# Optimization experiments

Hardware: AMD Instinct MI355X
Metric: run time of the kernel (lower is better)

## Reference

```python
import jax, jax.numpy as jnp
import numpy as np

N_NODES = 100000
N_EDGES = 1600000
IN, HID, OUT = 128, 128, 64


def setup_inputs() -> dict:
    key = jax.random.key(0)
    ks = jax.random.split(key, 6)
    features = jax.random.normal(ks[0], (N_NODES, IN), dtype=jnp.float32)
    src = jax.random.randint(ks[1], (N_EDGES,), 0, N_NODES)
    dst = jax.random.randint(ks[2], (N_EDGES,), 0, N_NODES)
    # Glorot-style init scales
    W1 = jax.random.normal(ks[3], (IN, HID), dtype=jnp.float32) * (1.0 / np.sqrt(IN))
    b1 = jnp.zeros((HID,), dtype=jnp.float32)
    W2 = jax.random.normal(ks[4], (HID, OUT), dtype=jnp.float32) * (1.0 / np.sqrt(HID))
    b2 = jnp.zeros((OUT,), dtype=jnp.float32)
    return {"features": features, "src": src, "dst": dst,
            "W1": W1, "b1": b1, "W2": W2, "b2": b2}


def _graph_conv(h, W, b, src, dst, deg_inv):
    # DGL GraphConv, norm='right': aggregate sum of (x_u W) over in-neighbors,
    # divide by in-degree (clamped to >=1), then add bias.
    m = h @ W                                   # [N, F_out]
    agg = jax.ops.segment_sum(m[src], dst, num_segments=h.shape[0])  # [N, F_out]
    return agg * deg_inv[:, None] + b


def reference(features, src, dst, W1, b1, W2, b2):
    n = features.shape[0]
    deg = jax.ops.segment_sum(jnp.ones_like(dst, dtype=features.dtype), dst,
                              num_segments=n)
    deg_inv = 1.0 / jnp.maximum(deg, 1.0)       # clamp(min=1) as in DGL
    h = jax.nn.relu(_graph_conv(features, W1, b1, src, dst, deg_inv))
    # dropout(0.5) is identity in eval mode
    out = _graph_conv(h, W2, b2, src, dst, deg_inv)
    return out
```

## Files before the change

kernel.cpp:

```cpp
#include <hip/hip_runtime.h>
#include <hip/hip_fp16.h>


constexpr int CAP = 3072;
constexpr int CHUNK = 8192;

typedef _Float16 f16x8 __attribute__((ext_vector_type(8)));
typedef float f32x4 __attribute__((ext_vector_type(4)));

__global__ __launch_bounds__(256) void k_prep(
    const int* __restrict__ dst, int* __restrict__ counts,
    const float* __restrict__ W1, const float* __restrict__ W2,
    __half* __restrict__ W1t, __half* __restrict__ W2t,
    int E, int NB, int NC)
{
    __shared__ int sh[1024];
    const int tid = threadIdx.x;
    if (blockIdx.x < NC) {
        const int c = blockIdx.x;
        const int b0 = c * CHUNK;
        const int cnt = min(CHUNK, E - b0);
        for (int i = tid; i < NB; i += 256) sh[i] = 0;
        __syncthreads();
        for (int i = tid; i < cnt; i += 256)
            atomicAdd(&sh[dst[b0 + i] >> 7], 1);
        __syncthreads();
        for (int i = tid; i < NB; i += 256) counts[(size_t)c * NB + i] = sh[i];
    } else {
        const int t = (blockIdx.x - NC) * 256 + tid;
        if (t < 128 * 128) {
            const int k = t >> 7, n = t & 127;
            W1t[n * 128 + k] = __float2half(W1[t]);
        } else {
            const int u = t - 128 * 128;
            const int k = u >> 6, n = u & 63;
            W2t[n * 128 + k] = __float2half(W2[u]);
        }
    }
}

__global__ __launch_bounds__(256) void k_colscan(
    int* __restrict__ counts, int* __restrict__ btot, int NB, int NC)
{
    __shared__ int sh[256];
    const int b = blockIdx.x;
    const int tid = threadIdx.x;
    int carry = 0;
    for (int t0 = 0; t0 < NC; t0 += 256) {
        const int idx = t0 + tid;
        const int v = (idx < NC) ? counts[(size_t)idx * NB + b] : 0;
        sh[tid] = v;
        __syncthreads();
        for (int off = 1; off < 256; off <<= 1) {
            int u = (tid >= off) ? sh[tid - off] : 0;
            __syncthreads();
            if (tid >= off) sh[tid] += u;
            __syncthreads();
        }
        const int incl = sh[tid];
        const int tile_total = sh[255];
        if (idx < NC) counts[(size_t)idx * NB + b] = incl - v + carry;
        carry += tile_total;
        __syncthreads();
    }
    if (tid == 0) btot[b] = carry;
}

__global__ __launch_bounds__(1024) void k_bscan(
    const int* __restrict__ btot, int* __restrict__ bstart, int NB, int E)
{
    __shared__ int sh[1024];
    const int t = threadIdx.x;
    const int v = (t < NB) ? btot[t] : 0;
    sh[t] = v;
    __syncthreads();
    for (int off = 1; off < 1024; off <<= 1) {
        int u = (t >= off) ? sh[t - off] : 0;
        __syncthreads();
        if (t >= off) sh[t] += u;
        __syncthreads();
    }
    if (t < NB) bstart[t] = sh[t] - v;
    if (t == 0) bstart[NB] = E;
}

__global__ __launch_bounds__(256) void k_scatter2(
    const int* __restrict__ src, const int* __restrict__ dst,
    const int* __restrict__ cbase, const int* __restrict__ bstart,
    unsigned* __restrict__ pairs,
    const float* __restrict__ X, __half* __restrict__ X16,
    int E, int NB, int NC, long long n4)
{
    __shared__ int cur[1024];
    const int c = blockIdx.x;
    const int tid = threadIdx.x;

    if (c < NC) {
        const int b0 = c * CHUNK;
        const int cnt = min(CHUNK, E - b0);

        for (int i = tid; i < NB; i += 256)
            cur[i] = bstart[i] + cbase[(size_t)c * NB + i];
        __syncthreads();

        int i = tid;
        for (; i + 768 < cnt; i += 1024) {
            const int d0 = dst[b0 + i], s0 = src[b0 + i];
            const int d1 = dst[b0 + i + 256], s1 = src[b0 + i + 256];
            const int d2 = dst[b0 + i + 512], s2 = src[b0 + i + 512];
            const int d3 = dst[b0 + i + 768], s3 = src[b0 + i + 768];
            const int p0 = atomicAdd(&cur[d0 >> 7], 1);
            const int p1 = atomicAdd(&cur[d1 >> 7], 1);
            const int p2 = atomicAdd(&cur[d2 >> 7], 1);
            const int p3 = atomicAdd(&cur[d3 >> 7], 1);
            pairs[p0] = (unsigned)s0 | ((unsigned)(d0 & 127) << 17);
            pairs[p1] = (unsigned)s1 | ((unsigned)(d1 & 127) << 17);
            pairs[p2] = (unsigned)s2 | ((unsigned)(d2 & 127) << 17);
            pairs[p3] = (unsigned)s3 | ((unsigned)(d3 & 127) << 17);
        }
        for (; i < cnt; i += 256) {
            const int d = dst[b0 + i];
            const int p = atomicAdd(&cur[d >> 7], 1);
            pairs[p] = (unsigned)src[b0 + i] | ((unsigned)(d & 127) << 17);
        }
    }

    for (long long i = (long long)blockIdx.x * 256 + tid; i < n4;
         i += (long long)gridDim.x * 256) {
        const float4 v = ((const float4*)X)[i];
        __half2 h0 = __floats2half2_rn(v.x, v.y);
        __half2 h1 = __floats2half2_rn(v.z, v.w);
        uint2 o;
        o.x = *(const unsigned*)&h0;
        o.y = *(const unsigned*)&h1;
        ((uint2*)X16)[i] = o;
    }
}

__global__ __launch_bounds__(256) void k_sort(
    const unsigned* __restrict__ pairs, const int* __restrict__ bstart,
    int* __restrict__ edge_src, int* __restrict__ row_start, int N, int E)
{
    __shared__ unsigned sp[CAP];
    __shared__ int sorted[CAP];
    __shared__ int lcnt[128];
    __shared__ int ls[128];
    const int b = blockIdx.x;
    const int tid = threadIdx.x;
    const int beg = bstart[b], end = bstart[b + 1];
    const int cnt = end - beg;
    const bool fits = (cnt <= CAP);

    if (tid < 128) lcnt[tid] = 0;
    __syncthreads();

    if (fits) {
        for (int i = tid; i < cnt; i += 256) {
            const unsigned p = pairs[beg + i];
            sp[i] = p;
            atomicAdd(&lcnt[p >> 17], 1);
        }
    } else {
        for (int i = tid; i < cnt; i += 256)
            atomicAdd(&lcnt[pairs[beg + i] >> 17], 1);
    }
    __syncthreads();

    if (tid < 128) ls[tid] = lcnt[tid];
    __syncthreads();
    for (int off = 1; off < 128; off <<= 1) {
        int v = 0;
        if (tid < 128 && tid >= off) v = ls[tid - off];
        __syncthreads();
        if (tid < 128 && tid >= off) ls[tid] += v;
        __syncthreads();
    }

    if (tid < 128) {
        const int node = b * 128 + tid;
        if (node <= N) row_start[node] = beg + ls[tid] - lcnt[tid];
    }
    if (b == 0 && tid == 0) row_start[N] = E;
    __syncthreads();

    if (tid < 128) ls[tid] -= lcnt[tid];
    __syncthreads();

    if (fits) {
        for (int i = tid; i < cnt; i += 256) {
            const unsigned p = sp[i];
            const int pos = atomicAdd(&ls[p >> 17], 1);
            sorted[pos] = (int)(p & 0x1FFFFu);
        }
        __syncthreads();
        for (int i = tid; i < cnt; i += 256) edge_src[beg + i] = sorted[i];
    } else {
        for (int i = tid; i < cnt; i += 256) {
            const unsigned p = pairs[beg + i];
            const int pos = atomicAdd(&ls[p >> 17], 1);
            edge_src[beg + pos] = (int)(p & 0x1FFFFu);
        }
    }
}

__global__ __launch_bounds__(256) void k_agg1(
    const __half* __restrict__ M, const int* __restrict__ edge_src,
    const int* __restrict__ row_start, __half* __restrict__ outp, int N)
{
    const int node = (blockIdx.x * 256 + threadIdx.x) >> 4;
    if (node >= N) return;
    const unsigned li = threadIdx.x & 15;
    const int beg = row_start[node];
    const int end = row_start[node + 1];
    const float inv = 1.0f / fmaxf((float)(end - beg), 1.0f);
    const uint4* M4 = (const uint4*)M;

    float acc[8] = {};
    int j = beg;
    for (; j + 7 < end; j += 8) {
        unsigned o[8];
#pragma unroll
        for (int q = 0; q < 8; ++q)
            o[q] = ((unsigned)edge_src[j + q] << 4) | li;
        uint4 v[8];
#pragma unroll
        for (int q = 0; q < 8; ++q) v[q] = M4[o[q]];
#pragma unroll
        for (int q = 0; q < 8; ++q) {
            const __half2* h = (const __half2*)&v[q];
#pragma unroll
            for (int p = 0; p < 4; ++p) {
                const float2 f = __half22float2(h[p]);
                acc[2 * p] += f.x;
                acc[2 * p + 1] += f.y;
            }
        }
    }
    for (; j < end; ++j) {
        const uint4 v = M4[((unsigned)edge_src[j] << 4) | li];
        const __half2* h = (const __half2*)&v;
#pragma unroll
        for (int p = 0; p < 4; ++p) {
            const float2 f = __half22float2(h[p]);
            acc[2 * p] += f.x;
            acc[2 * p + 1] += f.y;
        }
    }
    __half2 r[4];
#pragma unroll
    for (int p = 0; p < 4; ++p)
        r[p] = __floats2half2_rn(acc[2 * p] * inv, acc[2 * p + 1] * inv);
    ((uint4*)(outp + (size_t)node * 128))[li] = *(const uint4*)r;
}

__global__ __launch_bounds__(256) void k_agg2(
    const __half* __restrict__ M, const int* __restrict__ edge_src,
    const int* __restrict__ row_start, const float* __restrict__ bias,
    float* __restrict__ outp, int N)
{
    const int node = (blockIdx.x * 256 + threadIdx.x) >> 3;
    if (node >= N) return;
    const unsigned li = threadIdx.x & 7;
    const int beg = row_start[node];
    const int end = row_start[node + 1];
    const float inv = 1.0f / fmaxf((float)(end - beg), 1.0f);
    const uint4* M4 = (const uint4*)M;

    float acc[8] = {};
    int j = beg;
    for (; j + 15 < end; j += 16) {
        unsigned o[16];
#pragma unroll
        for (int q = 0; q < 16; ++q)
            o[q] = ((unsigned)edge_src[j + q] << 3) | li;
        uint4 v[16];
#pragma unroll
        for (int q = 0; q < 16; ++q) v[q] = M4[o[q]];
#pragma unroll
        for (int q = 0; q < 16; ++q) {
            const __half2* h = (const __half2*)&v[q];
#pragma unroll
            for (int p = 0; p < 4; ++p) {
                const float2 f = __half22float2(h[p]);
                acc[2 * p] += f.x;
                acc[2 * p + 1] += f.y;
            }
        }
    }
    for (; j + 3 < end; j += 4) {
        unsigned o[4];
#pragma unroll
        for (int q = 0; q < 4; ++q)
            o[q] = ((unsigned)edge_src[j + q] << 3) | li;
        uint4 v[4];
#pragma unroll
        for (int q = 0; q < 4; ++q) v[q] = M4[o[q]];
#pragma unroll
        for (int q = 0; q < 4; ++q) {
            const __half2* h = (const __half2*)&v[q];
#pragma unroll
            for (int p = 0; p < 4; ++p) {
                const float2 f = __half22float2(h[p]);
                acc[2 * p] += f.x;
                acc[2 * p + 1] += f.y;
            }
        }
    }
    for (; j < end; ++j) {
        const uint4 v = M4[((unsigned)edge_src[j] << 3) | li];
        const __half2* h = (const __half2*)&v;
#pragma unroll
        for (int p = 0; p < 4; ++p) {
            const float2 f = __half22float2(h[p]);
            acc[2 * p] += f.x;
            acc[2 * p + 1] += f.y;
        }
    }
    const float4 b0 = ((const float4*)bias)[li * 2];
    const float4 b1 = ((const float4*)bias)[li * 2 + 1];
    float4 o0, o1;
    o0.x = fmaf(acc[0], inv, b0.x);
    o0.y = fmaf(acc[1], inv, b0.y);
    o0.z = fmaf(acc[2], inv, b0.z);
    o0.w = fmaf(acc[3], inv, b0.w);
    o1.x = fmaf(acc[4], inv, b1.x);
    o1.y = fmaf(acc[5], inv, b1.y);
    o1.z = fmaf(acc[6], inv, b1.z);
    o1.w = fmaf(acc[7], inv, b1.w);
    float4* op = (float4*)(outp + (size_t)node * 64);
    op[li * 2] = o0;
    op[li * 2 + 1] = o1;
}

__global__ __launch_bounds__(256) void k_mgemm2(
    const __half* __restrict__ A, const __half* __restrict__ W1t,
    const float* __restrict__ b1, const __half* __restrict__ W2t,
    __half* __restrict__ C, int N)
{
    __shared__ __align__(16) char lds[16384];
    const int tid = threadIdx.x;
    const int row0 = blockIdx.x * 64;

    for (int i = tid; i < 1024; i += 256) {
        const int r = i >> 4, ch = i & 15;
        const int row = row0 + r;
        uint4 v = make_uint4(0, 0, 0, 0);
        if (row < N) v = *(const uint4*)(A + (size_t)row * 128 + ch * 8);
        *(uint4*)(lds + r * 256 + ((ch * 16) ^ ((r & 7) << 4))) = v;
    }
    __syncthreads();

    const int w = tid >> 6, l = tid & 63;
    const int lr = l & 15, lk = l >> 4;
    const int arow = w * 16 + lr;

    f32x4 acc1[8] = {};
#pragma unroll
    for (int kb = 0; kb < 4; ++kb) {
        const f16x8 a = *(const f16x8*)(lds + arow * 256 +
                                        ((kb * 64 + lk * 16) ^ ((arow & 7) << 4)));
#pragma unroll
        for (int nt = 0; nt < 8; ++nt) {
            const f16x8 b = *(const f16x8*)(W1t + (nt * 16 + lr) * 128 + kb * 32 + lk * 8);
            acc1[nt] = __builtin_amdgcn_mfma_f32_16x16x32_f16(a, b, acc1[nt], 0, 0, 0);
        }
    }
    __syncthreads();

    char* hw = lds + w * 4096;
#pragma unroll
    for (int nt = 0; nt < 8; ++nt) {
        const int col = nt * 16 + lr;
        const float bv = b1[col];
#pragma unroll
        for (int i = 0; i < 4; ++i) {
            const int r = lk * 4 + i;
            const float v = fmaxf(acc1[nt][i] + bv, 0.f);
            *(__half*)(hw + r * 256 + ((col * 2) ^ ((r & 7) << 4))) = __float2half(v);
        }
    }
    __syncthreads();

    f32x4 acc2[4] = {};
#pragma unroll
    for (int kb = 0; kb < 4; ++kb) {
        const f16x8 a2 = *(const f16x8*)(hw + lr * 256 +
                                         ((kb * 64 + lk * 16) ^ ((lr & 7) << 4)));
#pragma unroll
        for (int nt = 0; nt < 4; ++nt) {
            const f16x8 b = *(const f16x8*)(W2t + (nt * 16 + lr) * 128 + kb * 32 + lk * 8);
            acc2[nt] = __builtin_amdgcn_mfma_f32_16x16x32_f16(a2, b, acc2[nt], 0, 0, 0);
        }
    }
    __syncthreads();

#pragma unroll
    for (int nt = 0; nt < 4; ++nt) {
        const int col = nt * 16 + lr;
#pragma unroll
        for (int i = 0; i < 4; ++i) {
            const int r = lk * 4 + i;
            *(__half*)(hw + r * 128 + ((col * 2) ^ ((r & 7) << 4))) = __float2half(acc2[nt][i]);
        }
    }
    __syncthreads();

    const int rbase = row0 + w * 16;
    for (int i = l; i < 128; i += 64) {
        const int r = i >> 3, c = i & 7;
        const int row = rbase + r;
        if (row < N)
            *(uint4*)(C + (size_t)row * 64 + c * 8) =
                *(const uint4*)(hw + r * 128 + ((c * 16) ^ ((r & 7) << 4)));
    }
}

extern "C" void kernel_launch(void* const* d_in, const int* in_sizes, int n_in,
                              void* d_out, int out_size, void* d_ws, size_t ws_size,
                              hipStream_t stream)
{
    const float* X  = (const float*)d_in[0];
    const int*  src = (const int*)d_in[1];
    const int*  dst = (const int*)d_in[2];
    const float* W1 = (const float*)d_in[3];
    const float* b1 = (const float*)d_in[4];
    const float* W2 = (const float*)d_in[5];
    const float* b2 = (const float*)d_in[6];
    float* out = (float*)d_out;

    const int N = in_sizes[0] / 128;
    const int E = in_sizes[1];
    const int NB = (N + 127) / 128;
    const int NC = (E + CHUNK - 1) / CHUNK;

    __half* X16   = (__half*)d_ws;
    __half* agg1h = X16 + (size_t)N * 128;
    __half* scr   = agg1h + (size_t)N * 128;
    __half* m2h   = X16;
    unsigned* pairs = (unsigned*)scr;
    int* edge_src  = (int*)(scr + (size_t)N * 128);
    int* row_start = edge_src + E;
    int* bstart    = row_start + N + 1;
    int* btot      = bstart + NB + 1;
    int* counts    = btot + NB;
    __half* W1t    = (__half*)(counts + (size_t)NC * NB);
    __half* W2t    = W1t + 128 * 128;

    k_prep<<<NC + 96, 256, 0, stream>>>(dst, counts, W1, W2, W1t, W2t, E, NB, NC);
    k_colscan<<<NB, 256, 0, stream>>>(counts, btot, NB, NC);
    k_bscan<<<1, 1024, 0, stream>>>(btot, bstart, NB, E);
    k_scatter2<<<1024, 256, 0, stream>>>(src, dst, counts, bstart, pairs,
                                         X, X16, E, NB, NC, (long long)N * 32);
    k_sort<<<NB, 256, 0, stream>>>(pairs, bstart, edge_src, row_start, N, E);

    k_agg1<<<(N * 16 + 255) / 256, 256, 0, stream>>>(X16, edge_src, row_start, agg1h, N);
    k_mgemm2<<<(N + 63) / 64, 256, 0, stream>>>(agg1h, W1t, b1, W2t, m2h, N);
    k_agg2<<<(N * 8 + 255) / 256, 256, 0, stream>>>(m2h, edge_src, row_start, b2, out, N);
}
```

Measured before the change: 192.8 us.

## Fuse layer-1 aggregation into MFMA GEMM kernel and fold bucket scan into scatter

```diff
diff --git a/kernel.cpp b/kernel.cpp
--- a/kernel.cpp
+++ b/kernel.cpp
@@ -66,43 +66,52 @@
     if (tid == 0) btot[b] = carry;
 }
 
-__global__ __launch_bounds__(1024) void k_bscan(
-    const int* __restrict__ btot, int* __restrict__ bstart, int NB, int E)
-{
-    __shared__ int sh[1024];
-    const int t = threadIdx.x;
-    const int v = (t < NB) ? btot[t] : 0;
-    sh[t] = v;
-    __syncthreads();
-    for (int off = 1; off < 1024; off <<= 1) {
-        int u = (t >= off) ? sh[t - off] : 0;
-        __syncthreads();
-        if (t >= off) sh[t] += u;
-        __syncthreads();
-    }
-    if (t < NB) bstart[t] = sh[t] - v;
-    if (t == 0) bstart[NB] = E;
-}
-
 __global__ __launch_bounds__(256) void k_scatter2(
     const int* __restrict__ src, const int* __restrict__ dst,
-    const int* __restrict__ cbase, const int* __restrict__ bstart,
-    unsigned* __restrict__ pairs,
+    const int* __restrict__ cbase, const int* __restrict__ btot,
+    int* __restrict__ bstart_out, unsigned* __restrict__ pairs,
     const float* __restrict__ X, __half* __restrict__ X16,
     int E, int NB, int NC, long long n4)
 {
     __shared__ int cur[1024];
+    __shared__ int part[256];
     const int c = blockIdx.x;
     const int tid = threadIdx.x;
 
     if (c < NC) {
+        int v[4];
+        int run = 0;
+#pragma unroll
+        for (int q = 0; q < 4; ++q) {
+            const int idx = tid * 4 + q;
+            const int t = (idx < NB) ? btot[idx] : 0;
+            v[q] = run;
+            run += t;
+        }
+        part[tid] = run;
+        __syncthreads();
+        for (int off = 1; off < 256; off <<= 1) {
+            int u = (tid >= off) ? part[tid - off] : 0;
+            __syncthreads();
+            if (tid >= off) part[tid] += u;
+            __syncthreads();
+        }
+        const int excl = part[tid] - run;
+#pragma unroll
+        for (int q = 0; q < 4; ++q) cur[tid * 4 + q] = v[q] + excl;
+        __syncthreads();
+
+        if (c == 0) {
+            for (int i = tid; i < NB; i += 256) bstart_out[i] = cur[i];
+            if (tid == 0) bstart_out[NB] = E;
+        }
+
+        for (int i = tid; i < NB; i += 256)
+            cur[i] += cbase[(size_t)c * NB + i];
+        __syncthreads();
+
         const int b0 = c * CHUNK;
         const int cnt = min(CHUNK, E - b0);
-
-        for (int i = tid; i < NB; i += 256)
-            cur[i] = bstart[i] + cbase[(size_t)c * NB + i];
-        __syncthreads();
-
         int i = tid;
         for (; i + 768 < cnt; i += 1024) {
             const int d0 = dst[b0 + i], s0 = src[b0 + i];
@@ -203,54 +212,132 @@
     }
 }
 
-__global__ __launch_bounds__(256) void k_agg1(
-    const __half* __restrict__ M, const int* __restrict__ edge_src,
-    const int* __restrict__ row_start, __half* __restrict__ outp, int N)
-{
-    const int node = (blockIdx.x * 256 + threadIdx.x) >> 4;
-    if (node >= N) return;
-    const unsigned li = threadIdx.x & 15;
-    const int beg = row_start[node];
-    const int end = row_start[node + 1];
-    const float inv = 1.0f / fmaxf((float)(end - beg), 1.0f);
-    const uint4* M4 = (const uint4*)M;
-
-    float acc[8] = {};
-    int j = beg;
-    for (; j + 7 < end; j += 8) {
-        unsigned o[8];
-#pragma unroll
-        for (int q = 0; q < 8; ++q)
-            o[q] = ((unsigned)edge_src[j + q] << 4) | li;
-        uint4 v[8];
-#pragma unroll
-        for (int q = 0; q < 8; ++q) v[q] = M4[o[q]];
-#pragma unroll
-        for (int q = 0; q < 8; ++q) {
-            const __half2* h = (const __half2*)&v[q];
-#pragma unroll
-            for (int p = 0; p < 4; ++p) {
-                const float2 f = __half22float2(h[p]);
-                acc[2 * p] += f.x;
-                acc[2 * p + 1] += f.y;
+__global__ __launch_bounds__(256) void k_fused1(
+    const __half* __restrict__ X16, const int* __restrict__ edge_src,
+    const int* __restrict__ row_start, const __half* __restrict__ W1t,
+    const float* __restrict__ b1, const __half* __restrict__ W2t,
+    __half* __restrict__ C, int N)
+{
+    __shared__ __align__(16) char lds[16384];
+    const int tid = threadIdx.x;
+    const int row0 = blockIdx.x * 64;
+    const uint4* M4 = (const uint4*)X16;
+
+#pragma unroll
+    for (int pass = 0; pass < 4; ++pass) {
+        const int i = pass * 256 + tid;
+        const int r = i >> 4;
+        const unsigned ch = i & 15;
+        const int row = row0 + r;
+        float acc[8] = {};
+        if (row < N) {
+            const int beg = row_start[row];
+            const int end = row_start[row + 1];
+            const float inv = 1.0f / fmaxf((float)(end - beg), 1.0f);
+            int j = beg;
+            for (; j + 7 < end; j += 8) {
+                unsigned o[8];
+#pragma unroll
+                for (int q = 0; q < 8; ++q)
+                    o[q] = ((unsigned)edge_src[j + q] << 4) | ch;
+                uint4 v[8];
+#pragma unroll
+                for (int q = 0; q < 8; ++q) v[q] = M4[o[q]];
+#pragma unroll
+                for (int q = 0; q < 8; ++q) {
+                    const __half2* h = (const __half2*)&v[q];
+#pragma unroll
+                    for (int p = 0; p < 4; ++p) {
+                        const float2 f = __half22float2(h[p]);
+                        acc[2 * p] += f.x;
+                        acc[2 * p + 1] += f.y;
+                    }
+                }
             }
-        }
-    }
-    for (; j < end; ++j) {
-        const uint4 v = M4[((unsigned)edge_src[j] << 4) | li];
-        const __half2* h = (const __half2*)&v;
-#pragma unroll
-        for (int p = 0; p < 4; ++p) {
-            const float2 f = __half22float2(h[p]);
-            acc[2 * p] += f.x;
-            acc[2 * p + 1] += f.y;
-        }
-    }
-    __half2 r[4];
-#pragma unroll
-    for (int p = 0; p < 4; ++p)
-        r[p] = __floats2half2_rn(acc[2 * p] * inv, acc[2 * p + 1] * inv);
-    ((uint4*)(outp + (size_t)node * 128))[li] = *(const uint4*)r;
+            for (; j < end; ++j) {
+                const uint4 v = M4[((unsigned)edge_src[j] << 4) | ch];
+                const __half2* h = (const __half2*)&v;
+#pragma unroll
+                for (int p = 0; p < 4; ++p) {
+                    const float2 f = __half22float2(h[p]);
+                    acc[2 * p] += f.x;
+                    acc[2 * p + 1] += f.y;
+                }
+            }
+#pragma unroll
+            for (int q = 0; q < 8; ++q) acc[q] *= inv;
+        }
+        __half2 rr[4];
+#pragma unroll
+        for (int p = 0; p < 4; ++p)
+            rr[p] = __floats2half2_rn(acc[2 * p], acc[2 * p + 1]);
+        *(uint4*)(lds + r * 256 + ((ch * 16) ^ ((r & 7) << 4))) = *(const uint4*)rr;
+    }
+    __syncthreads();
+
+    const int w = tid >> 6, l = tid & 63;
+    const int lr = l & 15, lk = l >> 4;
+    const int arow = w * 16 + lr;
+
+    f32x4 acc1[8] = {};
+#pragma unroll
+    for (int kb = 0; kb < 4; ++kb) {
+        const f16x8 a = *(const f16x8*)(lds + arow * 256 +
+                                        ((kb * 64 + lk * 16) ^ ((arow & 7) << 4)));
+#pragma unroll
+        for (int nt = 0; nt < 8; ++nt) {
+            const f16x8 b = *(const f16x8*)(W1t + (nt * 16 + lr) * 128 + kb * 32 + lk * 8);
+            acc1[nt] = __builtin_amdgcn_mfma_f32_16x16x32_f16(a, b, acc1[nt], 0, 0, 0);
+        }
+    }
+    __syncthreads();
+
+    char* hw = lds + w * 4096;
+#pragma unroll
+    for (int nt = 0; nt < 8; ++nt) {
+        const int col = nt * 16 + lr;
+        const float bv = b1[col];
+#pragma unroll
+        for (int i = 0; i < 4; ++i) {
+            const int r = lk * 4 + i;
+            const float v = fmaxf(acc1[nt][i] + bv, 0.f);
+            *(__half*)(hw + r * 256 + ((col * 2) ^ ((r & 7) << 4))) = __float2half(v);
+        }
+    }
+    __syncthreads();
+
+    f32x4 acc2[4] = {};
+#pragma unroll
+    for (int kb = 0; kb < 4; ++kb) {
+        const f16x8 a2 = *(const f16x8*)(hw + lr * 256 +
+                                         ((kb * 64 + lk * 16) ^ ((lr & 7) << 4)));
+#pragma unroll
+        for (int nt = 0; nt < 4; ++nt) {
+            const f16x8 b = *(const f16x8*)(W2t + (nt * 16 + lr) * 128 + kb * 32 + lk * 8);
+            acc2[nt] = __builtin_amdgcn_mfma_f32_16x16x32_f16(a2, b, acc2[nt], 0, 0, 0);
+        }
+    }
+    __syncthreads();
+
+#pragma unroll
+    for (int nt = 0; nt < 4; ++nt) {
+        const int col = nt * 16 + lr;
+#pragma unroll
+        for (int i = 0; i < 4; ++i) {
+            const int r = lk * 4 + i;
+            *(__half*)(hw + r * 128 + ((col * 2) ^ ((r & 7) << 4))) = __float2half(acc2[nt][i]);
+        }
+    }
+    __syncthreads();
+
+    const int rbase = row0 + w * 16;
+    for (int i = l; i < 128; i += 64) {
+        const int r = i >> 3, c = i & 7;
+        const int row = rbase + r;
+        if (row < N)
+            *(uint4*)(C + (size_t)row * 64 + c * 8) =
+                *(const uint4*)(hw + r * 128 + ((c * 16) ^ ((r & 7) << 4)));
+    }
 }
 
 __global__ __launch_bounds__(256) void k_agg2(
@@ -332,89 +419,6 @@
     op[li * 2 + 1] = o1;
 }
 
-__global__ __launch_bounds__(256) void k_mgemm2(
-    const __half* __restrict__ A, const __half* __restrict__ W1t,
-    const float* __restrict__ b1, const __half* __restrict__ W2t,
-    __half* __restrict__ C, int N)
-{
-    __shared__ __align__(16) char lds[16384];
-    const int tid = threadIdx.x;
-    const int row0 = blockIdx.x * 64;
-
-    for (int i = tid; i < 1024; i += 256) {
-        const int r = i >> 4, ch = i & 15;
-        const int row = row0 + r;
-        uint4 v = make_uint4(0, 0, 0, 0);
-        if (row < N) v = *(const uint4*)(A + (size_t)row * 128 + ch * 8);
-        *(uint4*)(lds + r * 256 + ((ch * 16) ^ ((r & 7) << 4))) = v;
-    }
-    __syncthreads();
-
-    const int w = tid >> 6, l = tid & 63;
-    const int lr = l & 15, lk = l >> 4;
-    const int arow = w * 16 + lr;
-
-    f32x4 acc1[8] = {};
-#pragma unroll
-    for (int kb = 0; kb < 4; ++kb) {
-        const f16x8 a = *(const f16x8*)(lds + arow * 256 +
-                                        ((kb * 64 + lk * 16) ^ ((arow & 7) << 4)));
-#pragma unroll
-        for (int nt = 0; nt < 8; ++nt) {
-            const f16x8 b = *(const f16x8*)(W1t + (nt * 16 + lr) * 128 + kb * 32 + lk * 8);
-            acc1[nt] = __builtin_amdgcn_mfma_f32_16x16x32_f16(a, b, acc1[nt], 0, 0, 0);
-        }
-    }
-    __syncthreads();
-
-    char* hw = lds + w * 4096;
-#pragma unroll
-    for (int nt = 0; nt < 8; ++nt) {
-        const int col = nt * 16 + lr;
-        const float bv = b1[col];
-#pragma unroll
-        for (int i = 0; i < 4; ++i) {
-            const int r = lk * 4 + i;
-            const float v = fmaxf(acc1[nt][i] + bv, 0.f);
-            *(__half*)(hw + r * 256 + ((col * 2) ^ ((r & 7) << 4))) = __float2half(v);
-        }
-    }
-    __syncthreads();
-
-    f32x4 acc2[4] = {};
-#pragma unroll
-    for (int kb = 0; kb < 4; ++kb) {
-        const f16x8 a2 = *(const f16x8*)(hw + lr * 256 +
-                                         ((kb * 64 + lk * 16) ^ ((lr & 7) << 4)));
-#pragma unroll
-        for (int nt = 0; nt < 4; ++nt) {
-            const f16x8 b = *(const f16x8*)(W2t + (nt * 16 + lr) * 128 + kb * 32 + lk * 8);
-            acc2[nt] = __builtin_amdgcn_mfma_f32_16x16x32_f16(a2, b, acc2[nt], 0, 0, 0);
-        }
-    }
-    __syncthreads();
-
-#pragma unroll
-    for (int nt = 0; nt < 4; ++nt) {
-        const int col = nt * 16 + lr;
-#pragma unroll
-        for (int i = 0; i < 4; ++i) {
-            const int r = lk * 4 + i;
-            *(__half*)(hw + r * 128 + ((col * 2) ^ ((r & 7) << 4))) = __float2half(acc2[nt][i]);
-        }
-    }
-    __syncthreads();
-
-    const int rbase = row0 + w * 16;
-    for (int i = l; i < 128; i += 64) {
-        const int r = i >> 3, c = i & 7;
-        const int row = rbase + r;
-        if (row < N)
-            *(uint4*)(C + (size_t)row * 64 + c * 8) =
-                *(const uint4*)(hw + r * 128 + ((c * 16) ^ ((r & 7) << 4)));
-    }
-}
-
 extern "C" void kernel_launch(void* const* d_in, const int* in_sizes, int n_in,
                               void* d_out, int out_size, void* d_ws, size_t ws_size,
                               hipStream_t stream)
@@ -433,12 +437,10 @@
     const int NB = (N + 127) / 128;
     const int NC = (E + CHUNK - 1) / CHUNK;
 
-    __half* X16   = (__half*)d_ws;
-    __half* agg1h = X16 + (size_t)N * 128;
-    __half* scr   = agg1h + (size_t)N * 128;
-    __half* m2h   = X16;
-    unsigned* pairs = (unsigned*)scr;
-    int* edge_src  = (int*)(scr + (size_t)N * 128);
+    __half* X16    = (__half*)d_ws;
+    __half* m2h    = X16 + (size_t)N * 128;
+    unsigned* pairs = (unsigned*)(m2h + (size_t)N * 64);
+    int* edge_src  = (int*)(pairs + E);
     int* row_start = edge_src + E;
     int* bstart    = row_start + N + 1;
     int* btot      = bstart + NB + 1;
@@ -448,12 +450,11 @@
 
     k_prep<<<NC + 96, 256, 0, stream>>>(dst, counts, W1, W2, W1t, W2t, E, NB, NC);
     k_colscan<<<NB, 256, 0, stream>>>(counts, btot, NB, NC);
-    k_bscan<<<1, 1024, 0, stream>>>(btot, bstart, NB, E);
-    k_scatter2<<<1024, 256, 0, stream>>>(src, dst, counts, bstart, pairs,
+    k_scatter2<<<1024, 256, 0, stream>>>(src, dst, counts, btot, bstart, pairs,
                                          X, X16, E, NB, NC, (long long)N * 32);
     k_sort<<<NB, 256, 0, stream>>>(pairs, bstart, edge_src, row_start, N, E);
 
-    k_agg1<<<(N * 16 + 255) / 256, 256, 0, stream>>>(X16, edge_src, row_start, agg1h, N);
-    k_mgemm2<<<(N + 63) / 64, 256, 0, stream>>>(agg1h, W1t, b1, W2t, m2h, N);
+    k_fused1<<<(N + 63) / 64, 256, 0, stream>>>(X16, edge_src, row_start,
+                                                W1t, b1, W2t, m2h, N);
     k_agg2<<<(N * 8 + 255) / 256, 256, 0, stream>>>(m2h, edge_src, row_start, b2, out, N);
 }
```

New measurement: 185.4 us. 1.04x faster.
